# Optimization experiments

Measured on AMD Instinct MI355X. Metric: run time of the kernel, lower is better.

## Reference

```python
import jax, jax.numpy as jnp
import numpy as np

B, T, D, DO = 8, 2048, 1024, 1024

def setup_inputs() -> dict:
    key = jax.random.key(0)
    ks = jax.random.split(key, 7)
    s = 1.0 / np.sqrt(D)
    return {
        "input_tensor": jax.random.normal(ks[0], (B, T, D), dtype=jnp.float32),
        "Wq": jax.random.uniform(ks[1], (D, D), jnp.float32, -s, s),
        "bq": jax.random.uniform(ks[2], (D,), jnp.float32, -s, s),
        "Wk": jax.random.uniform(ks[3], (D, D), jnp.float32, -s, s),
        "bk": jax.random.uniform(ks[4], (D,), jnp.float32, -s, s),
        "Wv": jax.random.uniform(ks[5], (D, DO), jnp.float32, -s, s),
        "bv": jax.random.uniform(ks[6], (DO,), jnp.float32, -s, s),
    }

def reference(input_tensor, Wq, bq, Wk, bk, Wv, bv):
    scale = jnp.sqrt(jnp.float32(input_tensor.shape[-1]))
    q = input_tensor @ Wq + bq            # [B,T,D]
    k = input_tensor @ Wk + bk            # [B,T,D]
    v = input_tensor @ Wv + bv            # [B,T,DO]
    scores = jnp.einsum('btd,bsd->bts', q, k) / scale  # [B,T,T]
    attn = jax.nn.softmax(scores, axis=-1)
    return jnp.einsum('bts,bso->bto', attn, v)         # [B,T,DO]
```

## Files before the change

### kernel.cpp

```cpp
#include <hip/hip_runtime.h>
#include <stdint.h>

typedef unsigned short u16;
typedef __attribute__((ext_vector_type(4))) float    floatx4;
typedef __attribute__((ext_vector_type(8))) __bf16   bf16x8;
typedef __attribute__((ext_vector_type(2))) unsigned int uintx2;
typedef __attribute__((ext_vector_type(4))) unsigned int uintx4;

__device__ inline u16 f2bf(float f) {
  unsigned int u = __builtin_bit_cast(unsigned int, f);
  u += 0x7fffu + ((u >> 16) & 1u);
  return (u16)(u >> 16);
}

#define GLD16(gsrc, ldst)                                                        \
  __builtin_amdgcn_global_load_lds(                                              \
      (__attribute__((address_space(1))) void*)(gsrc),                           \
      (__attribute__((address_space(3))) void*)(ldst), 16, 0, 0)

__global__ __launch_bounds__(256) void prep_kernel(const float* __restrict__ x,
                                                   const float* __restrict__ Wq,
                                                   const float* __restrict__ Wk,
                                                   const float* __restrict__ Wv,
                                                   u16* __restrict__ xb,
                                                   u16* __restrict__ WT) {
  const int z = blockIdx.z;
  const int tid = threadIdx.y * 32 + threadIdx.x;
  if (z >= 3) {
    long blk = (long)(z - 3) * 1024 + blockIdx.y * 32 + blockIdx.x;
    long i = (blk * 256 + tid) * 8;
    floatx4 a = *(const floatx4*)(x + i);
    floatx4 b = *(const floatx4*)(x + i + 4);
    uintx4 o;
    o[0] = (unsigned)f2bf(a[0]) | ((unsigned)f2bf(a[1]) << 16);
    o[1] = (unsigned)f2bf(a[2]) | ((unsigned)f2bf(a[3]) << 16);
    o[2] = (unsigned)f2bf(b[0]) | ((unsigned)f2bf(b[1]) << 16);
    o[3] = (unsigned)f2bf(b[2]) | ((unsigned)f2bf(b[3]) << 16);
    *(uintx4*)(xb + i) = o;
    return;
  }
  __shared__ float tile[32][33];
  const float* W = (z == 0) ? Wq : (z == 1) ? Wk : Wv;
  u16* dst = WT + (long)z * 1024 * 1024;
  int bx = blockIdx.x * 32, by = blockIdx.y * 32;
  int tx = threadIdx.x, ty = threadIdx.y;
  for (int i = 0; i < 32; i += 8)
    tile[ty + i][tx] = W[(long)(by + ty + i) * 1024 + bx + tx];
  __syncthreads();
  for (int i = 0; i < 32; i += 8)
    dst[(long)(bx + ty + i) * 1024 + by + tx] = f2bf(tile[tx][ty + i]);
}

#define BM 256
#define BN 128
#define BK 64

template <int MODE, int GN>
__global__ __launch_bounds__(256, 2)
void gemm_bt(const u16* __restrict__ Aall, const u16* __restrict__ Ball,
             void* __restrict__ Call, void* __restrict__ C2,
             const float* __restrict__ bias, const float* __restrict__ bias2,
             float* __restrict__ lsum,
             int M, int N, int K, long aStride, long bStride, long cStride) {
  __shared__ __align__(16) u16 As[BM * BK];
  __shared__ __align__(16) u16 Bs[BN * BK];

  const int z = blockIdx.z;
  const u16* A  = Aall + (long)z * aStride;
  const u16* Bt = Ball + (long)z * bStride;

  int m_idx, n_idx;
  if (GN > 0) {
    const int tiles_n = gridDim.x, tiles_m = gridDim.y;
    int bid = blockIdx.y * tiles_n + blockIdx.x;
    int per_group = GN * tiles_m;
    int g = bid / per_group;
    int rem = bid - g * per_group;
    n_idx = g * GN + rem % GN;
    m_idx = rem / GN;
  } else {
    m_idx = blockIdx.y; n_idx = blockIdx.x;
  }

  const int tid  = threadIdx.x;
  const int m0   = m_idx * BM;
  const int n0   = n_idx * BN;
  const int wave = tid >> 6;
  const int lane = tid & 63;
  const int wm   = wave * 64;
  const int l15  = lane & 15;
  const int quad = lane >> 4;

  floatx4 acc[4][8];
  floatx4 zero = {0.f, 0.f, 0.f, 0.f};
#pragma unroll
  for (int i = 0; i < 4; ++i)
#pragma unroll
    for (int j = 0; j < 8; ++j) acc[i][j] = zero;

  int arow[8], acol[8];
  int brow[4], bcol[4];
#pragma unroll
  for (int i = 0; i < 8; ++i) {
    int ci = i * 256 + tid;
    int r = ci >> 3, sc = ci & 7;
    arow[i] = r; acol[i] = (sc ^ (r & 7)) * 8;
  }
#pragma unroll
  for (int i = 0; i < 4; ++i) {
    int ci = i * 256 + tid;
    int r = ci >> 3, sc = ci & 7;
    brow[i] = r; bcol[i] = (sc ^ (r & 7)) * 8;
  }

  for (int kt = 0; kt < K; kt += BK) {
#pragma unroll
    for (int i = 0; i < 8; ++i)
      GLD16(A + (long)(m0 + arow[i]) * K + kt + acol[i], As + (i * 256 + tid) * 8);
#pragma unroll
    for (int i = 0; i < 4; ++i)
      GLD16(Bt + (long)(n0 + brow[i]) * K + kt + bcol[i], Bs + (i * 256 + tid) * 8);
    __syncthreads();
#pragma unroll
    for (int ks = 0; ks < 2; ++ks) {
      bf16x8 af[4], bfr[8];
#pragma unroll
      for (int mi = 0; mi < 4; ++mi) {
        int r = wm + mi * 16 + l15;
        int ch = r * 8 + ((ks * 4 + quad) ^ (r & 7));
        af[mi] = *(const bf16x8*)(As + ch * 8);
      }
#pragma unroll
      for (int ni = 0; ni < 8; ++ni) {
        int r = ni * 16 + l15;
        int ch = r * 8 + ((ks * 4 + quad) ^ (r & 7));
        bfr[ni] = *(const bf16x8*)(Bs + ch * 8);
      }
#pragma unroll
      for (int mi = 0; mi < 4; ++mi)
#pragma unroll
        for (int ni = 0; ni < 8; ++ni)
          acc[mi][ni] = __builtin_amdgcn_mfma_f32_16x16x32_bf16(
              bfr[ni], af[mi], acc[mi][ni], 0, 0, 0);
    }
    __syncthreads();
  }

#pragma unroll
  for (int mi = 0; mi < 4; ++mi) {
    const int row = m0 + wm + mi * 16 + l15;
    if (MODE == 2) {
      u16* C = (u16*)Call + (long)z * cStride;
      float rs = 0.f;
#pragma unroll
      for (int ni = 0; ni < 8; ++ni) {
        int colb = n0 + ni * 16 + quad * 4;
        floatx4 v = acc[mi][ni];
        float e0 = __expf(v[0] * 0.03125f), e1 = __expf(v[1] * 0.03125f);
        float e2 = __expf(v[2] * 0.03125f), e3 = __expf(v[3] * 0.03125f);
        rs += (e0 + e1) + (e2 + e3);
        uintx2 o;
        o[0] = (unsigned)f2bf(e0) | ((unsigned)f2bf(e1) << 16);
        o[1] = (unsigned)f2bf(e2) | ((unsigned)f2bf(e3) << 16);
        *(uintx2*)(C + (long)row * N + colb) = o;
      }
      rs += __shfl_xor(rs, 16);
      rs += __shfl_xor(rs, 32);
      if (quad == 0) atomicAdd(lsum + (long)z * 2048 + row, rs);
    } else if (MODE == 3) {
      float* C = (float*)Call + (long)z * cStride;
      float inv = 1.0f / lsum[(long)z * 2048 + row];
#pragma unroll
      for (int ni = 0; ni < 8; ++ni) {
        int colb = n0 + ni * 16 + quad * 4;
        floatx4 v = acc[mi][ni];
        floatx4 o = {v[0] * inv, v[1] * inv, v[2] * inv, v[3] * inv};
        *(floatx4*)(C + (long)row * N + colb) = o;
      }
    } else if (MODE == 0) {
#pragma unroll
      for (int ni = 0; ni < 8; ++ni) {
        int colb = n0 + ni * 16 + quad * 4;
        u16* C = (colb < 1024) ? (u16*)Call : (u16*)C2;
        const float* bp = (colb < 1024) ? bias + colb : bias2 + (colb - 1024);
        floatx4 b = *(const floatx4*)bp;
        floatx4 v = acc[mi][ni];
        uintx2 o;
        o[0] = (unsigned)f2bf(v[0] + b[0]) | ((unsigned)f2bf(v[1] + b[1]) << 16);
        o[1] = (unsigned)f2bf(v[2] + b[2]) | ((unsigned)f2bf(v[3] + b[3]) << 16);
        *(uintx2*)(C + (long)row * 1024 + (colb & 1023)) = o;
      }
    } else {
      u16* C = (u16*)Call;
      float b = bias[row];
#pragma unroll
      for (int ni = 0; ni < 8; ++ni) {
        int colb = n0 + ni * 16 + quad * 4;
        long base = ((long)(colb >> 11) * 1024) * 2048 + (colb & 2047);
        floatx4 v = acc[mi][ni];
        uintx2 o;
        o[0] = (unsigned)f2bf(v[0] + b) | ((unsigned)f2bf(v[1] + b) << 16);
        o[1] = (unsigned)f2bf(v[2] + b) | ((unsigned)f2bf(v[3] + b) << 16);
        *(uintx2*)(C + base + (long)row * 2048) = o;
      }
    }
  }
}

extern "C" void kernel_launch(void* const* d_in, const int* in_sizes, int n_in,
                              void* d_out, int out_size, void* d_ws, size_t ws_size,
                              hipStream_t stream) {
  const float* x  = (const float*)d_in[0];
  const float* Wq = (const float*)d_in[1];
  const float* bq = (const float*)d_in[2];
  const float* Wk = (const float*)d_in[3];
  const float* bk = (const float*)d_in[4];
  const float* Wv = (const float*)d_in[5];
  const float* bv = (const float*)d_in[6];
  float* out = (float*)d_out;

  const long BT = 16384;
  u16* xb = (u16*)d_ws;
  u16* WT = xb + BT * 1024;
  u16* qb = WT + 3L * 1024 * 1024;
  u16* kb = qb + BT * 1024;
  u16* vT = kb + BT * 1024;
  u16* S  = vT + BT * 1024;
  float* lsum = (float*)(S + 8L * 2048 * 2048);

  hipMemsetAsync(lsum, 0, 8 * 2048 * sizeof(float), stream);

  prep_kernel<<<dim3(32, 32, 11), dim3(32, 8), 0, stream>>>(x, Wq, Wk, Wv, xb, WT);

  gemm_bt<0, 8><<<dim3(16, 64, 1), 256, 0, stream>>>(
      xb, WT, qb, kb, bq, bk, nullptr, 16384, 2048, 1024, 0, 0, 0);
  gemm_bt<1, 8><<<dim3(128, 4, 1), 256, 0, stream>>>(
      WT + 2L * 1024 * 1024, xb, vT, nullptr, bv, nullptr, nullptr,
      1024, 16384, 1024, 0, 0, 0);
  gemm_bt<2, 8><<<dim3(16, 8, 8), 256, 0, stream>>>(
      qb, kb, S, nullptr, nullptr, nullptr, lsum,
      2048, 2048, 1024, 2048L * 1024, 2048L * 1024, 2048L * 2048);
  gemm_bt<3, 8><<<dim3(8, 8, 8), 256, 0, stream>>>(
      S, vT, out, nullptr, nullptr, nullptr, lsum,
      2048, 1024, 2048, 2048L * 2048, 1024L * 2048, 2048L * 1024);
}
```

Measured before the change: 423.3 us.

## Double-buffer GEMM LDS tiles with 256x256 blocks and 512-thread 2x4 wave grid

Grows the GEMM output tile to 256x256 with 8 waves arranged 2x4, and double-buffers the A/B LDS tiles. Global-to-LDS loads for tile t+2 are issued after the first half of tile t's MFMAs, with explicit vmcnt/lgkmcnt waits, barriers and setprio around the MFMA bursts. This overlaps memory traffic with compute and improves operand reuse per block. In exchange LDS use doubles to 128KB per block, which limits occupancy, and the grids shrink (e.g. 256 blocks for the final GEMM), which may leave some CUs idle.

```diff
diff --git a/kernel.cpp b/kernel.cpp
--- a/kernel.cpp
+++ b/kernel.cpp
@@ -52,18 +52,18 @@
 }
 
 #define BM 256
-#define BN 128
+#define BN 256
 #define BK 64
 
 template <int MODE, int GN>
-__global__ __launch_bounds__(256, 2)
+__global__ __launch_bounds__(512, 2)
 void gemm_bt(const u16* __restrict__ Aall, const u16* __restrict__ Ball,
              void* __restrict__ Call, void* __restrict__ C2,
              const float* __restrict__ bias, const float* __restrict__ bias2,
              float* __restrict__ lsum,
              int M, int N, int K, long aStride, long bStride, long cStride) {
-  __shared__ __align__(16) u16 As[BM * BK];
-  __shared__ __align__(16) u16 Bs[BN * BK];
+  __shared__ __align__(16) u16 As[2][BM * BK];
+  __shared__ __align__(16) u16 Bs[2][BN * BK];
 
   const int z = blockIdx.z;
   const u16* A  = Aall + (long)z * aStride;
@@ -87,74 +87,101 @@
   const int n0   = n_idx * BN;
   const int wave = tid >> 6;
   const int lane = tid & 63;
-  const int wm   = wave * 64;
+  const int wm   = (wave >> 2) * 128;
+  const int wn   = (wave & 3) * 64;
   const int l15  = lane & 15;
   const int quad = lane >> 4;
 
-  floatx4 acc[4][8];
+  floatx4 acc[8][4];
   floatx4 zero = {0.f, 0.f, 0.f, 0.f};
 #pragma unroll
-  for (int i = 0; i < 4; ++i)
-#pragma unroll
-    for (int j = 0; j < 8; ++j) acc[i][j] = zero;
-
-  int arow[8], acol[8];
-  int brow[4], bcol[4];
-#pragma unroll
-  for (int i = 0; i < 8; ++i) {
-    int ci = i * 256 + tid;
+  for (int i = 0; i < 8; ++i)
+#pragma unroll
+    for (int j = 0; j < 4; ++j) acc[i][j] = zero;
+
+  int rows[4], cols[4];
+#pragma unroll
+  for (int i = 0; i < 4; ++i) {
+    int ci = i * 512 + tid;
     int r = ci >> 3, sc = ci & 7;
-    arow[i] = r; acol[i] = (sc ^ (r & 7)) * 8;
-  }
-#pragma unroll
-  for (int i = 0; i < 4; ++i) {
-    int ci = i * 256 + tid;
-    int r = ci >> 3, sc = ci & 7;
-    brow[i] = r; bcol[i] = (sc ^ (r & 7)) * 8;
-  }
-
-  for (int kt = 0; kt < K; kt += BK) {
-#pragma unroll
-    for (int i = 0; i < 8; ++i)
-      GLD16(A + (long)(m0 + arow[i]) * K + kt + acol[i], As + (i * 256 + tid) * 8);
+    rows[i] = r; cols[i] = (sc ^ (r & 7)) * 8;
+  }
+
+  auto stage = [&](int kt, u16* as, u16* bs) {
 #pragma unroll
     for (int i = 0; i < 4; ++i)
-      GLD16(Bt + (long)(n0 + brow[i]) * K + kt + bcol[i], Bs + (i * 256 + tid) * 8);
-    __syncthreads();
-#pragma unroll
-    for (int ks = 0; ks < 2; ++ks) {
-      bf16x8 af[4], bfr[8];
-#pragma unroll
-      for (int mi = 0; mi < 4; ++mi) {
-        int r = wm + mi * 16 + l15;
-        int ch = r * 8 + ((ks * 4 + quad) ^ (r & 7));
-        af[mi] = *(const bf16x8*)(As + ch * 8);
-      }
-#pragma unroll
-      for (int ni = 0; ni < 8; ++ni) {
-        int r = ni * 16 + l15;
-        int ch = r * 8 + ((ks * 4 + quad) ^ (r & 7));
-        bfr[ni] = *(const bf16x8*)(Bs + ch * 8);
-      }
-#pragma unroll
-      for (int mi = 0; mi < 4; ++mi)
-#pragma unroll
-        for (int ni = 0; ni < 8; ++ni)
-          acc[mi][ni] = __builtin_amdgcn_mfma_f32_16x16x32_bf16(
-              bfr[ni], af[mi], acc[mi][ni], 0, 0, 0);
-    }
-    __syncthreads();
-  }
-
-#pragma unroll
-  for (int mi = 0; mi < 4; ++mi) {
+      GLD16(A + (long)(m0 + rows[i]) * K + kt + cols[i], as + (i * 512 + tid) * 8);
+#pragma unroll
+    for (int i = 0; i < 4; ++i)
+      GLD16(Bt + (long)(n0 + rows[i]) * K + kt + cols[i], bs + (i * 512 + tid) * 8);
+  };
+
+  const int nt = K / BK;
+  stage(0, As[0], Bs[0]);
+  stage(BK, As[1], Bs[1]);
+
+  for (int t = 0; t < nt; ++t) {
+    const int cur = t & 1;
+    const u16* Ab = As[cur];
+    const u16* Bb = Bs[cur];
+    if (t + 1 < nt) asm volatile("s_waitcnt vmcnt(8)" ::: "memory");
+    else            asm volatile("s_waitcnt vmcnt(0)" ::: "memory");
+    __builtin_amdgcn_s_barrier();
+    __builtin_amdgcn_sched_barrier(0);
+
+    bf16x8 af0[8], bf0[4], af1[8], bf1[4];
+#pragma unroll
+    for (int mi = 0; mi < 8; ++mi) {
+      int r = wm + mi * 16 + l15;
+      af0[mi] = *(const bf16x8*)(Ab + (r * 8 + (quad ^ (r & 7))) * 8);
+    }
+#pragma unroll
+    for (int ni = 0; ni < 4; ++ni) {
+      int r = wn + ni * 16 + l15;
+      bf0[ni] = *(const bf16x8*)(Bb + (r * 8 + (quad ^ (r & 7))) * 8);
+    }
+    __builtin_amdgcn_s_setprio(1);
+#pragma unroll
+    for (int mi = 0; mi < 8; ++mi)
+#pragma unroll
+      for (int ni = 0; ni < 4; ++ni)
+        acc[mi][ni] = __builtin_amdgcn_mfma_f32_16x16x32_bf16(
+            bf0[ni], af0[mi], acc[mi][ni], 0, 0, 0);
+    __builtin_amdgcn_s_setprio(0);
+#pragma unroll
+    for (int mi = 0; mi < 8; ++mi) {
+      int r = wm + mi * 16 + l15;
+      af1[mi] = *(const bf16x8*)(Ab + (r * 8 + ((4 + quad) ^ (r & 7))) * 8);
+    }
+#pragma unroll
+    for (int ni = 0; ni < 4; ++ni) {
+      int r = wn + ni * 16 + l15;
+      bf1[ni] = *(const bf16x8*)(Bb + (r * 8 + ((4 + quad) ^ (r & 7))) * 8);
+    }
+    asm volatile("s_waitcnt lgkmcnt(0)" ::: "memory");
+    __builtin_amdgcn_sched_barrier(0);
+    __builtin_amdgcn_s_barrier();
+    __builtin_amdgcn_sched_barrier(0);
+    if (t + 2 < nt) stage((t + 2) * BK, As[cur], Bs[cur]);
+    __builtin_amdgcn_s_setprio(1);
+#pragma unroll
+    for (int mi = 0; mi < 8; ++mi)
+#pragma unroll
+      for (int ni = 0; ni < 4; ++ni)
+        acc[mi][ni] = __builtin_amdgcn_mfma_f32_16x16x32_bf16(
+            bf1[ni], af1[mi], acc[mi][ni], 0, 0, 0);
+    __builtin_amdgcn_s_setprio(0);
+  }
+
+#pragma unroll
+  for (int mi = 0; mi < 8; ++mi) {
     const int row = m0 + wm + mi * 16 + l15;
     if (MODE == 2) {
       u16* C = (u16*)Call + (long)z * cStride;
       float rs = 0.f;
 #pragma unroll
-      for (int ni = 0; ni < 8; ++ni) {
-        int colb = n0 + ni * 16 + quad * 4;
+      for (int ni = 0; ni < 4; ++ni) {
+        int colb = n0 + wn + ni * 16 + quad * 4;
         floatx4 v = acc[mi][ni];
         float e0 = __expf(v[0] * 0.03125f), e1 = __expf(v[1] * 0.03125f);
         float e2 = __expf(v[2] * 0.03125f), e3 = __expf(v[3] * 0.03125f);
@@ -171,16 +198,16 @@
       float* C = (float*)Call + (long)z * cStride;
       float inv = 1.0f / lsum[(long)z * 2048 + row];
 #pragma unroll
-      for (int ni = 0; ni < 8; ++ni) {
-        int colb = n0 + ni * 16 + quad * 4;
+      for (int ni = 0; ni < 4; ++ni) {
+        int colb = n0 + wn + ni * 16 + quad * 4;
         floatx4 v = acc[mi][ni];
         floatx4 o = {v[0] * inv, v[1] * inv, v[2] * inv, v[3] * inv};
         *(floatx4*)(C + (long)row * N + colb) = o;
       }
     } else if (MODE == 0) {
 #pragma unroll
-      for (int ni = 0; ni < 8; ++ni) {
-        int colb = n0 + ni * 16 + quad * 4;
+      for (int ni = 0; ni < 4; ++ni) {
+        int colb = n0 + wn + ni * 16 + quad * 4;
         u16* C = (colb < 1024) ? (u16*)Call : (u16*)C2;
         const float* bp = (colb < 1024) ? bias + colb : bias2 + (colb - 1024);
         floatx4 b = *(const floatx4*)bp;
@@ -194,8 +221,8 @@
       u16* C = (u16*)Call;
       float b = bias[row];
 #pragma unroll
-      for (int ni = 0; ni < 8; ++ni) {
-        int colb = n0 + ni * 16 + quad * 4;
+      for (int ni = 0; ni < 4; ++ni) {
+        int colb = n0 + wn + ni * 16 + quad * 4;
         long base = ((long)(colb >> 11) * 1024) * 2048 + (colb & 2047);
         floatx4 v = acc[mi][ni];
         uintx2 o;
@@ -232,15 +259,15 @@
 
   prep_kernel<<<dim3(32, 32, 11), dim3(32, 8), 0, stream>>>(x, Wq, Wk, Wv, xb, WT);
 
-  gemm_bt<0, 8><<<dim3(16, 64, 1), 256, 0, stream>>>(
+  gemm_bt<0, 8><<<dim3(8, 64, 1), 512, 0, stream>>>(
       xb, WT, qb, kb, bq, bk, nullptr, 16384, 2048, 1024, 0, 0, 0);
-  gemm_bt<1, 8><<<dim3(128, 4, 1), 256, 0, stream>>>(
+  gemm_bt<1, 8><<<dim3(64, 4, 1), 512, 0, stream>>>(
       WT + 2L * 1024 * 1024, xb, vT, nullptr, bv, nullptr, nullptr,
       1024, 16384, 1024, 0, 0, 0);
-  gemm_bt<2, 8><<<dim3(16, 8, 8), 256, 0, stream>>>(
+  gemm_bt<2, 8><<<dim3(8, 8, 8), 512, 0, stream>>>(
       qb, kb, S, nullptr, nullptr, nullptr, lsum,
       2048, 2048, 1024, 2048L * 1024, 2048L * 1024, 2048L * 2048);
-  gemm_bt<3, 8><<<dim3(8, 8, 8), 256, 0, stream>>>(
+  gemm_bt<3, 4><<<dim3(4, 8, 8), 512, 0, stream>>>(
       S, vT, out, nullptr, nullptr, nullptr, lsum,
       2048, 1024, 2048, 2048L * 2048, 1024L * 2048, 2048L * 1024);
 }
```

After: 384.4 us. -9.2%, faster.
